# Kernel tuning notes

Measured on AMD Instinct MI355X. Metric: run time of the kernel, lower is better.

The kernel has to match this reference:

```python
import jax, jax.numpy as jnp
import numpy as np

C_IN = 64
C_QK = C_IN // 8  # 8


def setup_inputs() -> dict:
    key = jax.random.key(0)
    ks = jax.random.split(key, 8)
    B, C, D, H, W = 2, C_IN, 8, 32, 32
    x = jax.random.normal(ks[0], (B, C, D, H, W), dtype=jnp.float32)
    s = 1.0 / np.sqrt(C)
    Wq = jax.random.normal(ks[1], (C_QK, C), dtype=jnp.float32) * s
    bq = jax.random.normal(ks[2], (C_QK,), dtype=jnp.float32) * 0.01
    Wk = jax.random.normal(ks[3], (C_QK, C), dtype=jnp.float32) * s
    bk = jax.random.normal(ks[4], (C_QK,), dtype=jnp.float32) * 0.01
    Wv = jax.random.normal(ks[5], (C, C), dtype=jnp.float32) * s
    bv = jax.random.normal(ks[6], (C,), dtype=jnp.float32) * 0.01
    gamma = jax.random.normal(ks[7], (1,), dtype=jnp.float32) * 0.1
    return {"x": x, "Wq": Wq, "bq": bq, "Wk": Wk, "bk": bk,
            "Wv": Wv, "bv": bv, "gamma": gamma}


def reference(x, Wq, bq, Wk, bk, Wv, bv, gamma):
    B, C, D, H, W = x.shape
    N = D * H * W
    xf = x.reshape(B, C, N)  # flatten spatial dims (D,H,W order)
    # 1x1x1 conv3d == per-position channel matmul
    q = jnp.einsum('oc,bcn->bno', Wq, xf) + bq            # [B, N, Cqk]
    k = jnp.einsum('oc,bcn->bon', Wk, xf) + bk[:, None]   # [B, Cqk, N]
    v = jnp.einsum('oc,bcn->bon', Wv, xf) + bv[:, None]   # [B, C, N]
    energy = jnp.einsum('bnc,bcm->bnm', q, k)             # [B, N, N] (unscaled)
    attn = jax.nn.softmax(energy, axis=-1)
    # out[b,c,m] = sum_n v[b,c,n] * attn[b,m,n]  (bmm with attention^T)
    out = jnp.einsum('bcn,bmn->bcm', v, attn)
    out = out.reshape(B, C, D, H, W)
    return gamma[0] * out + x
```

## Files before the change

### kernel.cpp

```cpp
#include <hip/hip_runtime.h>
#include <hip/hip_bf16.h>
#include <math.h>

#define NPOS 8192
#define CIN 64
#define CQK 8
#define NB 2
#define LOG2E 1.4426950408889634f
#define SOFF 16.0f

typedef __attribute__((ext_vector_type(8))) short bf16x8;
typedef __attribute__((ext_vector_type(16))) float f32x16;

__device__ __forceinline__ unsigned short f2bf(float f) {
  union { float f; unsigned int u; } a; a.f = f;
  unsigned int r = a.u + 0x7FFFu + ((a.u >> 16) & 1u);
  return (unsigned short)(r >> 16);
}

__global__ __launch_bounds__(256) void qkv_proj(
    const float* __restrict__ x,
    const float* __restrict__ Wq, const float* __restrict__ bq,
    const float* __restrict__ Wk, const float* __restrict__ bk,
    const float* __restrict__ Wv, const float* __restrict__ bv,
    unsigned short* __restrict__ Qb, unsigned short* __restrict__ Kb,
    unsigned short* __restrict__ VB) {
  __shared__ float sWq[CQK * CIN], sWk[CQK * CIN], sWv[CIN * CIN], sb[2 * CQK + CIN];
  __shared__ unsigned short sV[64][66];
  int t = threadIdx.x;
  for (int i = t; i < CQK * CIN; i += 256) { sWq[i] = Wq[i] * LOG2E; sWk[i] = Wk[i]; }
  for (int i = t; i < CIN * CIN; i += 256) sWv[i] = Wv[i];
  if (t < CQK) sb[t] = bq[t] * LOG2E;
  if (t >= CQK && t < 2 * CQK) sb[t] = bk[t - CQK];
  if (t >= 2 * CQK && t < 2 * CQK + CIN) sb[t] = bv[t - 2 * CQK];
  __syncthreads();

  int p_loc = t & 63, grp = t >> 6;
  int gid = blockIdx.x * 64 + p_loc;
  int b = gid >> 13;
  int n = gid & (NPOS - 1);
  const float* xp = x + (size_t)b * CIN * NPOS + n;
  float xv[CIN];
#pragma unroll
  for (int c = 0; c < CIN; ++c) xv[c] = xp[(size_t)c * NPOS];

#pragma unroll
  for (int e = 0; e < 2; ++e) {
    int o = grp * 2 + e;
    float aq = sb[o], ak = sb[CQK + o];
    const float4* wq4 = (const float4*)&sWq[o * CIN];
    const float4* wk4 = (const float4*)&sWk[o * CIN];
#pragma unroll
    for (int c4 = 0; c4 < 16; ++c4) {
      float4 wq = wq4[c4], wk = wk4[c4];
      float x0 = xv[4 * c4], x1 = xv[4 * c4 + 1], x2 = xv[4 * c4 + 2], x3 = xv[4 * c4 + 3];
      aq += wq.x * x0 + wq.y * x1 + wq.z * x2 + wq.w * x3;
      ak += wk.x * x0 + wk.y * x1 + wk.z * x2 + wk.w * x3;
    }
    Qb[(size_t)gid * CQK + o] = f2bf(aq);
    Kb[(size_t)gid * CQK + o] = f2bf(ak);
  }
  for (int oo = 0; oo < 16; ++oo) {
    int o = grp * 16 + oo;
    float av = sb[2 * CQK + o];
    const float4* wv4 = (const float4*)&sWv[o * CIN];
#pragma unroll
    for (int c4 = 0; c4 < 16; ++c4) {
      float4 w = wv4[c4];
      av += w.x * xv[4 * c4] + w.y * xv[4 * c4 + 1] + w.z * xv[4 * c4 + 2] + w.w * xv[4 * c4 + 3];
    }
    sV[p_loc][o] = f2bf(av);
  }
  __syncthreads();

  int gid0 = blockIdx.x * 64;
  int bb = gid0 >> 13;
  int jb0 = (gid0 & (NPOS - 1)) >> 5;
  for (int cc = t; cc < 512; cc += 256) {
    int jbl = cc >> 8;
    int rem = cc & 255;
    int f = rem >> 6;
    int ln = rem & 63;
    int ch = ((f >> 1) << 5) + (ln & 31);
    int w0 = ((f & 1) << 4) + (((ln >> 5) & 1) << 2);
    union { unsigned short s[8]; bf16x8 v; } ou;
#pragma unroll
    for (int i = 0; i < 8; ++i) {
      int p = (jbl << 5) + w0 + (i & 3) + (((i >> 2) & 1) << 3);
      ou.s[i] = sV[p][ch];
    }
    *reinterpret_cast<bf16x8*>(
        VB + (((size_t)bb * 256 + jb0 + jbl) * 2048 + (size_t)f * 512 + ln * 8)) = ou.v;
  }
}

__global__ __launch_bounds__(512, 2) void flash_attn(
    const unsigned short* __restrict__ Qb, const unsigned short* __restrict__ Kb,
    const unsigned short* __restrict__ VB, const float* __restrict__ x,
    const float* __restrict__ gamma, float* __restrict__ out) {
  int tid = threadIdx.x;
  int wave = tid >> 6, lane = tid & 63;
  int qcol = lane & 31, hi = lane >> 5;
  int blk = blockIdx.x;
  int b = blk >> 8, qt = blk & 255;
  int qbase = qt * 32;

  bf16x8 qfrag;
#pragma unroll
  for (int i = 0; i < 8; ++i) qfrag[i] = 0;
  if (!hi) qfrag = *reinterpret_cast<const bf16x8*>(
      Qb + ((size_t)b * NPOS + qbase + qcol) * CQK);

  f32x16 z;
#pragma unroll
  for (int i = 0; i < 16; ++i) z[i] = -SOFF;
  f32x16 acc0, acc1;
#pragma unroll
  for (int i = 0; i < 16; ++i) { acc0[i] = 0.f; acc1[i] = 0.f; }
  float l = 0.f;

  const unsigned short* Kp = Kb + (size_t)b * NPOS * CQK;
  const bf16x8* Vt = reinterpret_cast<const bf16x8*>(VB + (size_t)b * 256 * 2048);

  int jb0 = wave << 5;
  bf16x8 kcur;
#pragma unroll
  for (int i = 0; i < 8; ++i) kcur[i] = 0;
  if (!hi) kcur = *reinterpret_cast<const bf16x8*>(
      Kp + ((size_t)(jb0 << 5) + qcol) * CQK);

  for (int t = 0; t < 32; ++t) {
    const bf16x8* tile = Vt + (size_t)(jb0 + t) * 256;
    bf16x8 va0 = tile[lane];
    bf16x8 va1 = tile[64 + lane];
    bf16x8 vb0 = tile[128 + lane];
    bf16x8 vb1 = tile[192 + lane];

    f32x16 S = __builtin_amdgcn_mfma_f32_32x32x16_bf16(kcur, qfrag, z, 0, 0, 0);

    bf16x8 knx;
#pragma unroll
    for (int i = 0; i < 8; ++i) knx[i] = 0;
    {
      int jn = jb0 + ((t + 1) & 31);
      if (!hi) knx = *reinterpret_cast<const bf16x8*>(
          Kp + ((size_t)(jn << 5) + qcol) * CQK);
    }

    unsigned int pk[8];
    float ls0 = 0.f, ls1 = 0.f;
#pragma unroll
    for (int jj = 0; jj < 8; ++jj) {
      float pa = __builtin_amdgcn_exp2f(S[2 * jj]);
      float pb = __builtin_amdgcn_exp2f(S[2 * jj + 1]);
      ls0 += pa; ls1 += pb;
      pk[jj] = __builtin_amdgcn_perm(__float_as_uint(pb), __float_as_uint(pa), 0x07060302u);
    }
    l += ls0 + ls1;

    union { unsigned int ui[4]; bf16x8 v; } PA0, PA1;
    PA0.ui[0] = pk[0]; PA0.ui[1] = pk[1]; PA0.ui[2] = pk[2]; PA0.ui[3] = pk[3];
    PA1.ui[0] = pk[4]; PA1.ui[1] = pk[5]; PA1.ui[2] = pk[6]; PA1.ui[3] = pk[7];

    acc0 = __builtin_amdgcn_mfma_f32_32x32x16_bf16(va0, PA0.v, acc0, 0, 0, 0);
    acc0 = __builtin_amdgcn_mfma_f32_32x32x16_bf16(va1, PA1.v, acc0, 0, 0, 0);
    acc1 = __builtin_amdgcn_mfma_f32_32x32x16_bf16(vb0, PA0.v, acc1, 0, 0, 0);
    acc1 = __builtin_amdgcn_mfma_f32_32x32x16_bf16(vb1, PA1.v, acc1, 0, 0, 0);

    kcur = knx;
  }

  __shared__ float sL[8][32], sLinv[32];
  __shared__ float sacc[64][32];
  for (int i = tid; i < CIN * 32; i += 512) (&sacc[0][0])[i] = 0.f;
  float lp = l + __shfl_xor(l, 32);
  if (!hi) sL[wave][qcol] = lp;
  __syncthreads();
  if (tid < 32) {
    float L = 0.f;
    for (int w2 = 0; w2 < 8; ++w2) L += sL[w2][tid];
    sLinv[tid] = 1.0f / L;
  }
  __syncthreads();
  for (int w2 = 0; w2 < 8; ++w2) {
    if (wave == w2) {
#pragma unroll
      for (int r = 0; r < 16; ++r) {
        int c = (r & 3) + ((r >> 2) << 3) + (hi << 2);
        sacc[c][qcol]      += acc0[r];
        sacc[c + 32][qcol] += acc1[r];
      }
    }
    __syncthreads();
  }
  float g = gamma[0];
  for (int i = tid; i < CIN * 32; i += 512) {
    int c = i >> 5, q = i & 31;
    size_t idx = ((size_t)b * CIN + c) * NPOS + qbase + q;
    out[idx] = g * sacc[c][q] * sLinv[q] + x[idx];
  }
}

extern "C" void kernel_launch(void* const* d_in, const int* in_sizes, int n_in,
                              void* d_out, int out_size, void* d_ws, size_t ws_size,
                              hipStream_t stream) {
  const float* x     = (const float*)d_in[0];
  const float* Wq    = (const float*)d_in[1];
  const float* bq    = (const float*)d_in[2];
  const float* Wk    = (const float*)d_in[3];
  const float* bk    = (const float*)d_in[4];
  const float* Wv    = (const float*)d_in[5];
  const float* bv    = (const float*)d_in[6];
  const float* gamma = (const float*)d_in[7];
  float* out = (float*)d_out;

  unsigned short* Qb = (unsigned short*)d_ws;
  unsigned short* Kb = Qb + (size_t)NB * NPOS * CQK;
  unsigned short* VB = Kb + (size_t)NB * NPOS * CQK;

  qkv_proj<<<dim3(NB * NPOS / 64), dim3(256), 0, stream>>>(
      x, Wq, bq, Wk, bk, Wv, bv, Qb, Kb, VB);
  flash_attn<<<dim3(NB * NPOS / 32), dim3(512), 0, stream>>>(
      Qb, Kb, VB, x, gamma, out);
}
```

Measured before the change: 49.77 us.

## Process 64 queries per block, reusing K/V tiles across two query fragments

The attention kernel now handles 64 queries per block with 4 waves instead of 32 queries with 8 waves. Each loaded K and V tile feeds two query fragments, which halves global V traffic per query and doubles MFMA work per load. The cross-wave reduction is rewritten to use float4 stores into a transposed, padded shared buffer. The projection kernel moves to 512 threads, so each thread computes fewer output channels. The trade-offs are more accumulator registers per thread, which may lower occupancy, and half as many attention blocks.

```diff
diff --git a/kernel.cpp b/kernel.cpp
--- a/kernel.cpp
+++ b/kernel.cpp
@@ -18,7 +18,7 @@
   return (unsigned short)(r >> 16);
 }
 
-__global__ __launch_bounds__(256) void qkv_proj(
+__global__ __launch_bounds__(512, 2) void qkv_proj(
     const float* __restrict__ x,
     const float* __restrict__ Wq, const float* __restrict__ bq,
     const float* __restrict__ Wk, const float* __restrict__ bk,
@@ -28,8 +28,8 @@
   __shared__ float sWq[CQK * CIN], sWk[CQK * CIN], sWv[CIN * CIN], sb[2 * CQK + CIN];
   __shared__ unsigned short sV[64][66];
   int t = threadIdx.x;
-  for (int i = t; i < CQK * CIN; i += 256) { sWq[i] = Wq[i] * LOG2E; sWk[i] = Wk[i]; }
-  for (int i = t; i < CIN * CIN; i += 256) sWv[i] = Wv[i];
+  for (int i = t; i < CQK * CIN; i += 512) { sWq[i] = Wq[i] * LOG2E; sWk[i] = Wk[i]; }
+  for (int i = t; i < CIN * CIN; i += 512) sWv[i] = Wv[i];
   if (t < CQK) sb[t] = bq[t] * LOG2E;
   if (t >= CQK && t < 2 * CQK) sb[t] = bk[t - CQK];
   if (t >= 2 * CQK && t < 2 * CQK + CIN) sb[t] = bv[t - 2 * CQK];
@@ -44,9 +44,8 @@
 #pragma unroll
   for (int c = 0; c < CIN; ++c) xv[c] = xp[(size_t)c * NPOS];
 
-#pragma unroll
-  for (int e = 0; e < 2; ++e) {
-    int o = grp * 2 + e;
+  {
+    int o = grp;
     float aq = sb[o], ak = sb[CQK + o];
     const float4* wq4 = (const float4*)&sWq[o * CIN];
     const float4* wk4 = (const float4*)&sWk[o * CIN];
@@ -60,8 +59,9 @@
     Qb[(size_t)gid * CQK + o] = f2bf(aq);
     Kb[(size_t)gid * CQK + o] = f2bf(ak);
   }
-  for (int oo = 0; oo < 16; ++oo) {
-    int o = grp * 16 + oo;
+#pragma unroll
+  for (int oo = 0; oo < 8; ++oo) {
+    int o = grp * 8 + oo;
     float av = sb[2 * CQK + o];
     const float4* wv4 = (const float4*)&sWv[o * CIN];
 #pragma unroll
@@ -76,7 +76,8 @@
   int gid0 = blockIdx.x * 64;
   int bb = gid0 >> 13;
   int jb0 = (gid0 & (NPOS - 1)) >> 5;
-  for (int cc = t; cc < 512; cc += 256) {
+  {
+    int cc = t;
     int jbl = cc >> 8;
     int rem = cc & 255;
     int f = rem >> 6;
@@ -94,7 +95,7 @@
   }
 }
 
-__global__ __launch_bounds__(512, 2) void flash_attn(
+__global__ __launch_bounds__(256, 2) void flash_attn(
     const unsigned short* __restrict__ Qb, const unsigned short* __restrict__ Kb,
     const unsigned short* __restrict__ VB, const float* __restrict__ x,
     const float* __restrict__ gamma, float* __restrict__ out) {
@@ -102,102 +103,130 @@
   int wave = tid >> 6, lane = tid & 63;
   int qcol = lane & 31, hi = lane >> 5;
   int blk = blockIdx.x;
-  int b = blk >> 8, qt = blk & 255;
-  int qbase = qt * 32;
-
-  bf16x8 qfrag;
-#pragma unroll
-  for (int i = 0; i < 8; ++i) qfrag[i] = 0;
-  if (!hi) qfrag = *reinterpret_cast<const bf16x8*>(
-      Qb + ((size_t)b * NPOS + qbase + qcol) * CQK);
+  int b = blk >> 7, qt = blk & 127;
+  int qbase = qt * 64;
+
+  bf16x8 qfrag0, qfrag1;
+#pragma unroll
+  for (int i = 0; i < 8; ++i) { qfrag0[i] = 0; qfrag1[i] = 0; }
+  if (!hi) {
+    qfrag0 = *reinterpret_cast<const bf16x8*>(Qb + ((size_t)b * NPOS + qbase + qcol) * CQK);
+    qfrag1 = *reinterpret_cast<const bf16x8*>(Qb + ((size_t)b * NPOS + qbase + 32 + qcol) * CQK);
+  }
 
   f32x16 z;
 #pragma unroll
   for (int i = 0; i < 16; ++i) z[i] = -SOFF;
-  f32x16 acc0, acc1;
-#pragma unroll
-  for (int i = 0; i < 16; ++i) { acc0[i] = 0.f; acc1[i] = 0.f; }
-  float l = 0.f;
+  f32x16 accA0, accB0, accA1, accB1;
+#pragma unroll
+  for (int i = 0; i < 16; ++i) { accA0[i] = 0.f; accB0[i] = 0.f; accA1[i] = 0.f; accB1[i] = 0.f; }
+  float l0 = 0.f, l1 = 0.f;
 
   const unsigned short* Kp = Kb + (size_t)b * NPOS * CQK;
   const bf16x8* Vt = reinterpret_cast<const bf16x8*>(VB + (size_t)b * 256 * 2048);
 
-  int jb0 = wave << 5;
+  int jb0 = wave << 6;
   bf16x8 kcur;
 #pragma unroll
   for (int i = 0; i < 8; ++i) kcur[i] = 0;
-  if (!hi) kcur = *reinterpret_cast<const bf16x8*>(
-      Kp + ((size_t)(jb0 << 5) + qcol) * CQK);
-
-  for (int t = 0; t < 32; ++t) {
-    const bf16x8* tile = Vt + (size_t)(jb0 + t) * 256;
+  if (!hi) kcur = *reinterpret_cast<const bf16x8*>(Kp + ((size_t)(jb0 << 5) + qcol) * CQK);
+
+  for (int tt = 0; tt < 64; ++tt) {
+    const bf16x8* tile = Vt + (size_t)(jb0 + tt) * 256;
     bf16x8 va0 = tile[lane];
     bf16x8 va1 = tile[64 + lane];
     bf16x8 vb0 = tile[128 + lane];
     bf16x8 vb1 = tile[192 + lane];
 
-    f32x16 S = __builtin_amdgcn_mfma_f32_32x32x16_bf16(kcur, qfrag, z, 0, 0, 0);
+    f32x16 S0 = __builtin_amdgcn_mfma_f32_32x32x16_bf16(kcur, qfrag0, z, 0, 0, 0);
+    f32x16 S1 = __builtin_amdgcn_mfma_f32_32x32x16_bf16(kcur, qfrag1, z, 0, 0, 0);
 
     bf16x8 knx;
 #pragma unroll
     for (int i = 0; i < 8; ++i) knx[i] = 0;
     {
-      int jn = jb0 + ((t + 1) & 31);
-      if (!hi) knx = *reinterpret_cast<const bf16x8*>(
-          Kp + ((size_t)(jn << 5) + qcol) * CQK);
-    }
-
-    unsigned int pk[8];
-    float ls0 = 0.f, ls1 = 0.f;
+      int jn = jb0 + ((tt + 1) & 63);
+      if (!hi) knx = *reinterpret_cast<const bf16x8*>(Kp + ((size_t)(jn << 5) + qcol) * CQK);
+    }
+
+    unsigned int pk0[8], pk1[8];
+    float lsa = 0.f, lsb = 0.f, lsc = 0.f, lsd = 0.f;
 #pragma unroll
     for (int jj = 0; jj < 8; ++jj) {
-      float pa = __builtin_amdgcn_exp2f(S[2 * jj]);
-      float pb = __builtin_amdgcn_exp2f(S[2 * jj + 1]);
-      ls0 += pa; ls1 += pb;
-      pk[jj] = __builtin_amdgcn_perm(__float_as_uint(pb), __float_as_uint(pa), 0x07060302u);
-    }
-    l += ls0 + ls1;
-
-    union { unsigned int ui[4]; bf16x8 v; } PA0, PA1;
-    PA0.ui[0] = pk[0]; PA0.ui[1] = pk[1]; PA0.ui[2] = pk[2]; PA0.ui[3] = pk[3];
-    PA1.ui[0] = pk[4]; PA1.ui[1] = pk[5]; PA1.ui[2] = pk[6]; PA1.ui[3] = pk[7];
-
-    acc0 = __builtin_amdgcn_mfma_f32_32x32x16_bf16(va0, PA0.v, acc0, 0, 0, 0);
-    acc0 = __builtin_amdgcn_mfma_f32_32x32x16_bf16(va1, PA1.v, acc0, 0, 0, 0);
-    acc1 = __builtin_amdgcn_mfma_f32_32x32x16_bf16(vb0, PA0.v, acc1, 0, 0, 0);
-    acc1 = __builtin_amdgcn_mfma_f32_32x32x16_bf16(vb1, PA1.v, acc1, 0, 0, 0);
+      float pa = __builtin_amdgcn_exp2f(S0[2 * jj]);
+      float pb = __builtin_amdgcn_exp2f(S0[2 * jj + 1]);
+      float pc = __builtin_amdgcn_exp2f(S1[2 * jj]);
+      float pd = __builtin_amdgcn_exp2f(S1[2 * jj + 1]);
+      lsa += pa; lsb += pb; lsc += pc; lsd += pd;
+      pk0[jj] = __builtin_amdgcn_perm(__float_as_uint(pb), __float_as_uint(pa), 0x07060302u);
+      pk1[jj] = __builtin_amdgcn_perm(__float_as_uint(pd), __float_as_uint(pc), 0x07060302u);
+    }
+    l0 += lsa + lsb;
+    l1 += lsc + lsd;
+
+    union { unsigned int ui[4]; bf16x8 v; } PA00, PA10, PA01, PA11;
+    PA00.ui[0] = pk0[0]; PA00.ui[1] = pk0[1]; PA00.ui[2] = pk0[2]; PA00.ui[3] = pk0[3];
+    PA10.ui[0] = pk0[4]; PA10.ui[1] = pk0[5]; PA10.ui[2] = pk0[6]; PA10.ui[3] = pk0[7];
+    PA01.ui[0] = pk1[0]; PA01.ui[1] = pk1[1]; PA01.ui[2] = pk1[2]; PA01.ui[3] = pk1[3];
+    PA11.ui[0] = pk1[4]; PA11.ui[1] = pk1[5]; PA11.ui[2] = pk1[6]; PA11.ui[3] = pk1[7];
+
+    accA0 = __builtin_amdgcn_mfma_f32_32x32x16_bf16(va0, PA00.v, accA0, 0, 0, 0);
+    accA0 = __builtin_amdgcn_mfma_f32_32x32x16_bf16(va1, PA10.v, accA0, 0, 0, 0);
+    accB0 = __builtin_amdgcn_mfma_f32_32x32x16_bf16(vb0, PA00.v, accB0, 0, 0, 0);
+    accB0 = __builtin_amdgcn_mfma_f32_32x32x16_bf16(vb1, PA10.v, accB0, 0, 0, 0);
+    accA1 = __builtin_amdgcn_mfma_f32_32x32x16_bf16(va0, PA01.v, accA1, 0, 0, 0);
+    accA1 = __builtin_amdgcn_mfma_f32_32x32x16_bf16(va1, PA11.v, accA1, 0, 0, 0);
+    accB1 = __builtin_amdgcn_mfma_f32_32x32x16_bf16(vb0, PA01.v, accB1, 0, 0, 0);
+    accB1 = __builtin_amdgcn_mfma_f32_32x32x16_bf16(vb1, PA11.v, accB1, 0, 0, 0);
 
     kcur = knx;
   }
 
-  __shared__ float sL[8][32], sLinv[32];
-  __shared__ float sacc[64][32];
-  for (int i = tid; i < CIN * 32; i += 512) (&sacc[0][0])[i] = 0.f;
-  float lp = l + __shfl_xor(l, 32);
-  if (!hi) sL[wave][qcol] = lp;
-  __syncthreads();
-  if (tid < 32) {
-    float L = 0.f;
-    for (int w2 = 0; w2 < 8; ++w2) L += sL[w2][tid];
+  __shared__ float sL[4][64];
+  __shared__ float sLinv[64];
+  __shared__ float sacc[64][68];
+  float lp0 = l0 + __shfl_xor(l0, 32);
+  float lp1 = l1 + __shfl_xor(l1, 32);
+  if (!hi) { sL[wave][qcol] = lp0; sL[wave][32 + qcol] = lp1; }
+  __syncthreads();
+  if (tid < 64) {
+    float L = sL[0][tid] + sL[1][tid] + sL[2][tid] + sL[3][tid];
     sLinv[tid] = 1.0f / L;
   }
-  __syncthreads();
-  for (int w2 = 0; w2 < 8; ++w2) {
+
+  for (int w2 = 0; w2 < 4; ++w2) {
+    __syncthreads();
     if (wave == w2) {
 #pragma unroll
-      for (int r = 0; r < 16; ++r) {
-        int c = (r & 3) + ((r >> 2) << 3) + (hi << 2);
-        sacc[c][qcol]      += acc0[r];
-        sacc[c + 32][qcol] += acc1[r];
+      for (int k = 0; k < 4; ++k) {
+        int c0 = (k << 3) + (hi << 2);
+        float4 cA0 = make_float4(accA0[4 * k], accA0[4 * k + 1], accA0[4 * k + 2], accA0[4 * k + 3]);
+        float4 cB0 = make_float4(accB0[4 * k], accB0[4 * k + 1], accB0[4 * k + 2], accB0[4 * k + 3]);
+        float4 cA1 = make_float4(accA1[4 * k], accA1[4 * k + 1], accA1[4 * k + 2], accA1[4 * k + 3]);
+        float4 cB1 = make_float4(accB1[4 * k], accB1[4 * k + 1], accB1[4 * k + 2], accB1[4 * k + 3]);
+        float4* pA0 = (float4*)&sacc[qcol][c0];
+        float4* pB0 = (float4*)&sacc[qcol][c0 + 32];
+        float4* pA1 = (float4*)&sacc[32 + qcol][c0];
+        float4* pB1 = (float4*)&sacc[32 + qcol][c0 + 32];
+        if (w2 == 0) { *pA0 = cA0; *pB0 = cB0; *pA1 = cA1; *pB1 = cB1; }
+        else {
+          float4 a = *pA0, bq_ = *pB0, c = *pA1, d = *pB1;
+          a.x += cA0.x; a.y += cA0.y; a.z += cA0.z; a.w += cA0.w;
+          bq_.x += cB0.x; bq_.y += cB0.y; bq_.z += cB0.z; bq_.w += cB0.w;
+          c.x += cA1.x; c.y += cA1.y; c.z += cA1.z; c.w += cA1.w;
+          d.x += cB1.x; d.y += cB1.y; d.z += cB1.z; d.w += cB1.w;
+          *pA0 = a; *pB0 = bq_; *pA1 = c; *pB1 = d;
+        }
       }
     }
-    __syncthreads();
-  }
+  }
+  __syncthreads();
+
   float g = gamma[0];
-  for (int i = tid; i < CIN * 32; i += 512) {
-    int c = i >> 5, q = i & 31;
+  for (int i = tid; i < CIN * 64; i += 256) {
+    int c = i >> 6, q = i & 63;
     size_t idx = ((size_t)b * CIN + c) * NPOS + qbase + q;
-    out[idx] = g * sacc[c][q] * sLinv[q] + x[idx];
+    out[idx] = g * sacc[q][c] * sLinv[q] + x[idx];
   }
 }
 
@@ -218,8 +247,8 @@
   unsigned short* Kb = Qb + (size_t)NB * NPOS * CQK;
   unsigned short* VB = Kb + (size_t)NB * NPOS * CQK;
 
-  qkv_proj<<<dim3(NB * NPOS / 64), dim3(256), 0, stream>>>(
+  qkv_proj<<<dim3(NB * NPOS / 64), dim3(512), 0, stream>>>(
       x, Wq, bq, Wk, bk, Wv, bv, Qb, Kb, VB);
-  flash_attn<<<dim3(NB * NPOS / 32), dim3(512), 0, stream>>>(
+  flash_attn<<<dim3(NB * NPOS / 64), dim3(256), 0, stream>>>(
       Qb, Kb, VB, x, gamma, out);
 }
```

After: 47.18 us. 5.2% less time.

## Split attention over key ranges with LDS-staged shared K/V and a merge kernel

Applied to the files above, without the earlier changes.

The attention kernel now assigns 256 queries per block (32 per wave) and splits the key dimension into four chunks across blocks. K and V tiles are staged into LDS with global_load_lds double buffering, so all eight waves share each tile instead of each wave reading its own. Partial unnormalized outputs and row sums go to a workspace, and a new merge kernel sums them, normalizes, and applies the gamma residual. The projection kernel also switches to 32 positions per block. The cost is extra global traffic for the partials, a third launch, and per-step block barriers.

```diff
diff --git a/kernel.cpp b/kernel.cpp
--- a/kernel.cpp
+++ b/kernel.cpp
@@ -8,9 +8,15 @@
 #define NB 2
 #define LOG2E 1.4426950408889634f
 #define SOFF 16.0f
+#define KSPL 4
+#define KH (NPOS / KSPL)
+#define STEPS (KH / 64)
 
 typedef __attribute__((ext_vector_type(8))) short bf16x8;
 typedef __attribute__((ext_vector_type(16))) float f32x16;
+
+typedef __attribute__((address_space(3))) void lds_void;
+typedef __attribute__((address_space(1))) const void glb_void;
 
 __device__ __forceinline__ unsigned short f2bf(float f) {
   union { float f; unsigned int u; } a; a.f = f;
@@ -18,7 +24,7 @@
   return (unsigned short)(r >> 16);
 }
 
-__global__ __launch_bounds__(256) void qkv_proj(
+__global__ __launch_bounds__(256, 2) void qkv_proj(
     const float* __restrict__ x,
     const float* __restrict__ Wq, const float* __restrict__ bq,
     const float* __restrict__ Wk, const float* __restrict__ bk,
@@ -26,7 +32,7 @@
     unsigned short* __restrict__ Qb, unsigned short* __restrict__ Kb,
     unsigned short* __restrict__ VB) {
   __shared__ float sWq[CQK * CIN], sWk[CQK * CIN], sWv[CIN * CIN], sb[2 * CQK + CIN];
-  __shared__ unsigned short sV[64][66];
+  __shared__ unsigned short sV[32][66];
   int t = threadIdx.x;
   for (int i = t; i < CQK * CIN; i += 256) { sWq[i] = Wq[i] * LOG2E; sWk[i] = Wk[i]; }
   for (int i = t; i < CIN * CIN; i += 256) sWv[i] = Wv[i];
@@ -35,8 +41,8 @@
   if (t >= 2 * CQK && t < 2 * CQK + CIN) sb[t] = bv[t - 2 * CQK];
   __syncthreads();
 
-  int p_loc = t & 63, grp = t >> 6;
-  int gid = blockIdx.x * 64 + p_loc;
+  int p_loc = t & 31, grp = t >> 5;
+  int gid = blockIdx.x * 32 + p_loc;
   int b = gid >> 13;
   int n = gid & (NPOS - 1);
   const float* xp = x + (size_t)b * CIN * NPOS + n;
@@ -44,9 +50,8 @@
 #pragma unroll
   for (int c = 0; c < CIN; ++c) xv[c] = xp[(size_t)c * NPOS];
 
-#pragma unroll
-  for (int e = 0; e < 2; ++e) {
-    int o = grp * 2 + e;
+  {
+    int o = grp;
     float aq = sb[o], ak = sb[CQK + o];
     const float4* wq4 = (const float4*)&sWq[o * CIN];
     const float4* wk4 = (const float4*)&sWk[o * CIN];
@@ -60,8 +65,9 @@
     Qb[(size_t)gid * CQK + o] = f2bf(aq);
     Kb[(size_t)gid * CQK + o] = f2bf(ak);
   }
-  for (int oo = 0; oo < 16; ++oo) {
-    int o = grp * 16 + oo;
+#pragma unroll
+  for (int oo = 0; oo < 8; ++oo) {
+    int o = grp * 8 + oo;
     float av = sb[2 * CQK + o];
     const float4* wv4 = (const float4*)&sWv[o * CIN];
 #pragma unroll
@@ -73,43 +79,46 @@
   }
   __syncthreads();
 
-  int gid0 = blockIdx.x * 64;
-  int bb = gid0 >> 13;
-  int jb0 = (gid0 & (NPOS - 1)) >> 5;
-  for (int cc = t; cc < 512; cc += 256) {
-    int jbl = cc >> 8;
-    int rem = cc & 255;
-    int f = rem >> 6;
-    int ln = rem & 63;
+  {
+    int gid0 = blockIdx.x * 32;
+    int bb = gid0 >> 13;
+    int jb = (gid0 & (NPOS - 1)) >> 5;
+    int f = t >> 6;
+    int ln = t & 63;
     int ch = ((f >> 1) << 5) + (ln & 31);
     int w0 = ((f & 1) << 4) + (((ln >> 5) & 1) << 2);
     union { unsigned short s[8]; bf16x8 v; } ou;
 #pragma unroll
     for (int i = 0; i < 8; ++i) {
-      int p = (jbl << 5) + w0 + (i & 3) + (((i >> 2) & 1) << 3);
+      int p = w0 + (i & 3) + (((i >> 2) & 1) << 3);
       ou.s[i] = sV[p][ch];
     }
     *reinterpret_cast<bf16x8*>(
-        VB + (((size_t)bb * 256 + jb0 + jbl) * 2048 + (size_t)f * 512 + ln * 8)) = ou.v;
+        VB + (((size_t)bb * 256 + jb) * 2048 + (size_t)f * 512 + ln * 8)) = ou.v;
   }
 }
 
 __global__ __launch_bounds__(512, 2) void flash_attn(
     const unsigned short* __restrict__ Qb, const unsigned short* __restrict__ Kb,
-    const unsigned short* __restrict__ VB, const float* __restrict__ x,
-    const float* __restrict__ gamma, float* __restrict__ out) {
+    const unsigned short* __restrict__ VB,
+    float* __restrict__ Opart, float* __restrict__ lpart) {
+  __shared__ unsigned short sbuf[2][4608];
+  __shared__ float sep[8][64][33];
+
   int tid = threadIdx.x;
   int wave = tid >> 6, lane = tid & 63;
   int qcol = lane & 31, hi = lane >> 5;
   int blk = blockIdx.x;
-  int b = blk >> 8, qt = blk & 255;
-  int qbase = qt * 32;
+  int qb = blk >> 2, ks = blk & 3;
+  int b = qb >> 5;
+  int kbase = ks * KH;
+  int jbBase = (ks * KH) >> 5;
 
   bf16x8 qfrag;
 #pragma unroll
   for (int i = 0; i < 8; ++i) qfrag[i] = 0;
   if (!hi) qfrag = *reinterpret_cast<const bf16x8*>(
-      Qb + ((size_t)b * NPOS + qbase + qcol) * CQK);
+      Qb + ((size_t)qb * 256 + wave * 32 + qcol) * CQK);
 
   f32x16 z;
 #pragma unroll
@@ -120,84 +129,106 @@
   float l = 0.f;
 
   const unsigned short* Kp = Kb + (size_t)b * NPOS * CQK;
-  const bf16x8* Vt = reinterpret_cast<const bf16x8*>(VB + (size_t)b * 256 * 2048);
-
-  int jb0 = wave << 5;
-  bf16x8 kcur;
-#pragma unroll
-  for (int i = 0; i < 8; ++i) kcur[i] = 0;
-  if (!hi) kcur = *reinterpret_cast<const bf16x8*>(
-      Kp + ((size_t)(jb0 << 5) + qcol) * CQK);
-
-  for (int t = 0; t < 32; ++t) {
-    const bf16x8* tile = Vt + (size_t)(jb0 + t) * 256;
-    bf16x8 va0 = tile[lane];
-    bf16x8 va1 = tile[64 + lane];
-    bf16x8 vb0 = tile[128 + lane];
-    bf16x8 vb1 = tile[192 + lane];
-
-    f32x16 S = __builtin_amdgcn_mfma_f32_32x32x16_bf16(kcur, qfrag, z, 0, 0, 0);
-
-    bf16x8 knx;
-#pragma unroll
-    for (int i = 0; i < 8; ++i) knx[i] = 0;
-    {
-      int jn = jb0 + ((t + 1) & 31);
-      if (!hi) knx = *reinterpret_cast<const bf16x8*>(
-          Kp + ((size_t)(jn << 5) + qcol) * CQK);
-    }
-
-    unsigned int pk[8];
-    float ls0 = 0.f, ls1 = 0.f;
-#pragma unroll
-    for (int jj = 0; jj < 8; ++jj) {
-      float pa = __builtin_amdgcn_exp2f(S[2 * jj]);
-      float pb = __builtin_amdgcn_exp2f(S[2 * jj + 1]);
-      ls0 += pa; ls1 += pb;
-      pk[jj] = __builtin_amdgcn_perm(__float_as_uint(pb), __float_as_uint(pa), 0x07060302u);
-    }
-    l += ls0 + ls1;
-
-    union { unsigned int ui[4]; bf16x8 v; } PA0, PA1;
-    PA0.ui[0] = pk[0]; PA0.ui[1] = pk[1]; PA0.ui[2] = pk[2]; PA0.ui[3] = pk[3];
-    PA1.ui[0] = pk[4]; PA1.ui[1] = pk[5]; PA1.ui[2] = pk[6]; PA1.ui[3] = pk[7];
-
-    acc0 = __builtin_amdgcn_mfma_f32_32x32x16_bf16(va0, PA0.v, acc0, 0, 0, 0);
-    acc0 = __builtin_amdgcn_mfma_f32_32x32x16_bf16(va1, PA1.v, acc0, 0, 0, 0);
-    acc1 = __builtin_amdgcn_mfma_f32_32x32x16_bf16(vb0, PA0.v, acc1, 0, 0, 0);
-    acc1 = __builtin_amdgcn_mfma_f32_32x32x16_bf16(vb1, PA1.v, acc1, 0, 0, 0);
-
-    kcur = knx;
-  }
-
-  __shared__ float sL[8][32], sLinv[32];
-  __shared__ float sacc[64][32];
-  for (int i = tid; i < CIN * 32; i += 512) (&sacc[0][0])[i] = 0.f;
-  float lp = l + __shfl_xor(l, 32);
-  if (!hi) sL[wave][qcol] = lp;
+  const unsigned short* VBb = VB + (size_t)b * 256 * 2048;
+
+  auto stage = [&](int buf, int step) {
+    const unsigned short* vsrc =
+        VBb + ((size_t)(jbBase + step * 2)) * 2048 + wave * 512 + lane * 8;
+    __builtin_amdgcn_global_load_lds((glb_void*)vsrc,
+                                     (lds_void*)&sbuf[buf][wave * 512], 16, 0, 0);
+    if (wave == 0) {
+      const unsigned short* ksrc = Kp + ((size_t)(kbase + step * 64)) * CQK + lane * 8;
+      __builtin_amdgcn_global_load_lds((glb_void*)ksrc,
+                                       (lds_void*)&sbuf[buf][4096], 16, 0, 0);
+    }
+  };
+
+  stage(0, 0);
   __syncthreads();
-  if (tid < 32) {
-    float L = 0.f;
-    for (int w2 = 0; w2 < 8; ++w2) L += sL[w2][tid];
-    sLinv[tid] = 1.0f / L;
-  }
-  __syncthreads();
-  for (int w2 = 0; w2 < 8; ++w2) {
-    if (wave == w2) {
-#pragma unroll
-      for (int r = 0; r < 16; ++r) {
-        int c = (r & 3) + ((r >> 2) << 3) + (hi << 2);
-        sacc[c][qcol]      += acc0[r];
-        sacc[c + 32][qcol] += acc1[r];
+
+  for (int step = 0; step < STEPS; ++step) {
+    int cur = step & 1;
+    if (step + 1 < STEPS) stage(cur ^ 1, step + 1);
+
+#pragma unroll
+    for (int u = 0; u < 2; ++u) {
+      bf16x8 kfrag = *reinterpret_cast<const bf16x8*>(
+          &sbuf[cur][4096 + u * 256 + qcol * 8]);
+      f32x16 S = __builtin_amdgcn_mfma_f32_32x32x16_bf16(kfrag, qfrag, z, 0, 0, 0);
+
+      const unsigned short* vb = &sbuf[cur][u * 2048];
+      bf16x8 va0 = *reinterpret_cast<const bf16x8*>(vb + (size_t)lane * 8);
+      bf16x8 va1 = *reinterpret_cast<const bf16x8*>(vb + 512 + (size_t)lane * 8);
+      bf16x8 vb0 = *reinterpret_cast<const bf16x8*>(vb + 1024 + (size_t)lane * 8);
+      bf16x8 vb1 = *reinterpret_cast<const bf16x8*>(vb + 1536 + (size_t)lane * 8);
+
+      unsigned int pk[8];
+      float ls0 = 0.f, ls1 = 0.f;
+#pragma unroll
+      for (int jj = 0; jj < 8; ++jj) {
+        float pa = __builtin_amdgcn_exp2f(S[2 * jj]);
+        float pb = __builtin_amdgcn_exp2f(S[2 * jj + 1]);
+        ls0 += pa; ls1 += pb;
+        pk[jj] = __builtin_amdgcn_perm(__float_as_uint(pb), __float_as_uint(pa),
+                                       0x07060302u);
       }
+      l += ls0 + ls1;
+
+      union { unsigned int ui[4]; bf16x8 v; } PA0, PA1;
+      PA0.ui[0] = pk[0]; PA0.ui[1] = pk[1]; PA0.ui[2] = pk[2]; PA0.ui[3] = pk[3];
+      PA1.ui[0] = pk[4]; PA1.ui[1] = pk[5]; PA1.ui[2] = pk[6]; PA1.ui[3] = pk[7];
+
+      acc0 = __builtin_amdgcn_mfma_f32_32x32x16_bf16(va0, PA0.v, acc0, 0, 0, 0);
+      acc0 = __builtin_amdgcn_mfma_f32_32x32x16_bf16(va1, PA1.v, acc0, 0, 0, 0);
+      acc1 = __builtin_amdgcn_mfma_f32_32x32x16_bf16(vb0, PA0.v, acc1, 0, 0, 0);
+      acc1 = __builtin_amdgcn_mfma_f32_32x32x16_bf16(vb1, PA1.v, acc1, 0, 0, 0);
     }
     __syncthreads();
   }
-  float g = gamma[0];
-  for (int i = tid; i < CIN * 32; i += 512) {
-    int c = i >> 5, q = i & 31;
-    size_t idx = ((size_t)b * CIN + c) * NPOS + qbase + q;
-    out[idx] = g * sacc[c][q] * sLinv[q] + x[idx];
+
+  float l2 = l + __shfl_xor(l, 32);
+  if (!hi) lpart[((qb << 2) + ks) * 256 + wave * 32 + qcol] = l2;
+
+#pragma unroll
+  for (int r = 0; r < 16; ++r) {
+    int c0 = (r & 3) + ((r >> 2) << 3) + (hi << 2);
+    sep[wave][c0][qcol] = acc0[r];
+    sep[wave][c0 + 32][qcol] = acc1[r];
+  }
+  float* Ob = Opart + (((size_t)(qb << 2) + ks) << 6) * 256;
+#pragma unroll
+  for (int cc = 0; cc < 32; ++cc) {
+    int c = (cc << 1) | hi;
+    Ob[(size_t)c * 256 + wave * 32 + qcol] = sep[wave][c][qcol];
+  }
+}
+
+__global__ __launch_bounds__(256) void pam_merge(
+    const float* __restrict__ Opart, const float* __restrict__ lpart,
+    const float* __restrict__ x, const float* __restrict__ gamma,
+    float* __restrict__ out) {
+  int blk = blockIdx.x;
+  int qb = blk >> 3, oct = blk & 7;
+  int t = threadIdx.x;
+  int ql = oct * 32 + (t & 31);
+  int cg = t >> 5;
+  int gq = qb * 256 + ql;
+  int b = gq >> 13, pos = gq & (NPOS - 1);
+
+  float L = 0.f;
+#pragma unroll
+  for (int ksv = 0; ksv < KSPL; ++ksv) L += lpart[((qb << 2) + ksv) * 256 + ql];
+  float gi = gamma[0] / L;
+
+#pragma unroll
+  for (int j = 0; j < 8; ++j) {
+    int c = cg * 8 + j;
+    float s = 0.f;
+#pragma unroll
+    for (int ksv = 0; ksv < KSPL; ++ksv)
+      s += Opart[((((size_t)(qb << 2) + ksv) << 6) + c) * 256 + ql];
+    size_t oidx = ((size_t)(b * CIN + c)) * NPOS + pos;
+    out[oidx] = s * gi + x[oidx];
   }
 }
 
@@ -214,12 +245,15 @@
   const float* gamma = (const float*)d_in[7];
   float* out = (float*)d_out;
 
-  unsigned short* Qb = (unsigned short*)d_ws;
-  unsigned short* Kb = Qb + (size_t)NB * NPOS * CQK;
-  unsigned short* VB = Kb + (size_t)NB * NPOS * CQK;
-
-  qkv_proj<<<dim3(NB * NPOS / 64), dim3(256), 0, stream>>>(
+  char* ws = (char*)d_ws;
+  unsigned short* Qb = (unsigned short*)(ws);
+  unsigned short* Kb = (unsigned short*)(ws + (256 << 10));
+  unsigned short* VB = (unsigned short*)(ws + (512 << 10));
+  float* Opart = (float*)(ws + (4 << 20));
+  float* lpart = (float*)(ws + (20 << 20));
+
+  qkv_proj<<<dim3(NB * NPOS / 32), dim3(256), 0, stream>>>(
       x, Wq, bq, Wk, bk, Wv, bv, Qb, Kb, VB);
-  flash_attn<<<dim3(NB * NPOS / 32), dim3(512), 0, stream>>>(
-      Qb, Kb, VB, x, gamma, out);
-}
+  flash_attn<<<dim3(64 * KSPL), dim3(512), 0, stream>>>(Qb, Kb, VB, Opart, lpart);
+  pam_merge<<<dim3(64 * 8), dim3(256), 0, stream>>>(Opart, lpart, x, gamma, out);
+}
```

Measured after the change: 58.29 us. 1.17x slower.

## Restructure QKV projection and attention epilogue, relax flash-attention launch bounds

Applied to the files above, without the earlier changes.

The projection kernel now runs 512 threads per block, one wave per Q/K output channel. Weights are read directly from global memory with wave-uniform indices, which replaces the shared-memory staging and its barrier. In the attention kernel, the K-fragment loads drop the upper-half-lane mask, since those lanes pair with zeroed Q anyway. The cross-wave accumulator reduction now writes float4 rows into a transposed, padded shared buffer, so the zero-initialisation pass is skipped. The minimum-blocks hint of 2 per CU is removed from launch bounds, which may let the compiler use more registers at the cost of occupancy.

```diff
diff --git a/kernel.cpp b/kernel.cpp
--- a/kernel.cpp
+++ b/kernel.cpp
@@ -18,25 +18,18 @@
   return (unsigned short)(r >> 16);
 }
 
-__global__ __launch_bounds__(256) void qkv_proj(
+__global__ __launch_bounds__(512) void qkv_proj(
     const float* __restrict__ x,
     const float* __restrict__ Wq, const float* __restrict__ bq,
     const float* __restrict__ Wk, const float* __restrict__ bk,
     const float* __restrict__ Wv, const float* __restrict__ bv,
     unsigned short* __restrict__ Qb, unsigned short* __restrict__ Kb,
     unsigned short* __restrict__ VB) {
-  __shared__ float sWq[CQK * CIN], sWk[CQK * CIN], sWv[CIN * CIN], sb[2 * CQK + CIN];
   __shared__ unsigned short sV[64][66];
-  int t = threadIdx.x;
-  for (int i = t; i < CQK * CIN; i += 256) { sWq[i] = Wq[i] * LOG2E; sWk[i] = Wk[i]; }
-  for (int i = t; i < CIN * CIN; i += 256) sWv[i] = Wv[i];
-  if (t < CQK) sb[t] = bq[t] * LOG2E;
-  if (t >= CQK && t < 2 * CQK) sb[t] = bk[t - CQK];
-  if (t >= 2 * CQK && t < 2 * CQK + CIN) sb[t] = bv[t - 2 * CQK];
-  __syncthreads();
-
-  int p_loc = t & 63, grp = t >> 6;
-  int gid = blockIdx.x * 64 + p_loc;
+  int tid = threadIdx.x;
+  int wave = __builtin_amdgcn_readfirstlane(tid >> 6);
+  int lane = tid & 63;
+  int gid = blockIdx.x * 64 + lane;
   int b = gid >> 13;
   int n = gid & (NPOS - 1);
   const float* xp = x + (size_t)b * CIN * NPOS + n;
@@ -44,39 +37,36 @@
 #pragma unroll
   for (int c = 0; c < CIN; ++c) xv[c] = xp[(size_t)c * NPOS];
 
-#pragma unroll
-  for (int e = 0; e < 2; ++e) {
-    int o = grp * 2 + e;
-    float aq = sb[o], ak = sb[CQK + o];
-    const float4* wq4 = (const float4*)&sWq[o * CIN];
-    const float4* wk4 = (const float4*)&sWk[o * CIN];
-#pragma unroll
-    for (int c4 = 0; c4 < 16; ++c4) {
-      float4 wq = wq4[c4], wk = wk4[c4];
-      float x0 = xv[4 * c4], x1 = xv[4 * c4 + 1], x2 = xv[4 * c4 + 2], x3 = xv[4 * c4 + 3];
-      aq += wq.x * x0 + wq.y * x1 + wq.z * x2 + wq.w * x3;
-      ak += wk.x * x0 + wk.y * x1 + wk.z * x2 + wk.w * x3;
-    }
-    Qb[(size_t)gid * CQK + o] = f2bf(aq);
-    Kb[(size_t)gid * CQK + o] = f2bf(ak);
-  }
-  for (int oo = 0; oo < 16; ++oo) {
-    int o = grp * 16 + oo;
-    float av = sb[2 * CQK + o];
-    const float4* wv4 = (const float4*)&sWv[o * CIN];
-#pragma unroll
-    for (int c4 = 0; c4 < 16; ++c4) {
-      float4 w = wv4[c4];
-      av += w.x * xv[4 * c4] + w.y * xv[4 * c4 + 1] + w.z * xv[4 * c4 + 2] + w.w * xv[4 * c4 + 3];
-    }
-    sV[p_loc][o] = f2bf(av);
+  {
+    const float* wq = Wq + wave * CIN;
+    const float* wk = Wk + wave * CIN;
+    float aq = 0.f, ak = 0.f;
+#pragma unroll
+    for (int c = 0; c < CIN; ++c) {
+      aq += wq[c] * xv[c];
+      ak += wk[c] * xv[c];
+    }
+    aq = (aq + bq[wave]) * LOG2E;
+    ak += bk[wave];
+    Qb[(size_t)gid * CQK + wave] = f2bf(aq);
+    Kb[(size_t)gid * CQK + wave] = f2bf(ak);
+  }
+#pragma unroll
+  for (int oo = 0; oo < 8; ++oo) {
+    int o = wave * 8 + oo;
+    const float* wv = Wv + o * CIN;
+    float av = bv[o];
+#pragma unroll
+    for (int c = 0; c < CIN; ++c) av += wv[c] * xv[c];
+    sV[lane][o] = f2bf(av);
   }
   __syncthreads();
 
-  int gid0 = blockIdx.x * 64;
-  int bb = gid0 >> 13;
-  int jb0 = (gid0 & (NPOS - 1)) >> 5;
-  for (int cc = t; cc < 512; cc += 256) {
+  {
+    int gid0 = blockIdx.x * 64;
+    int bb = gid0 >> 13;
+    int jb0 = (gid0 & (NPOS - 1)) >> 5;
+    int cc = tid;
     int jbl = cc >> 8;
     int rem = cc & 255;
     int f = rem >> 6;
@@ -94,7 +84,7 @@
   }
 }
 
-__global__ __launch_bounds__(512, 2) void flash_attn(
+__global__ __launch_bounds__(512) void flash_attn(
     const unsigned short* __restrict__ Qb, const unsigned short* __restrict__ Kb,
     const unsigned short* __restrict__ VB, const float* __restrict__ x,
     const float* __restrict__ gamma, float* __restrict__ out) {
@@ -123,14 +113,10 @@
   const bf16x8* Vt = reinterpret_cast<const bf16x8*>(VB + (size_t)b * 256 * 2048);
 
   int jb0 = wave << 5;
-  bf16x8 kcur;
-#pragma unroll
-  for (int i = 0; i < 8; ++i) kcur[i] = 0;
-  if (!hi) kcur = *reinterpret_cast<const bf16x8*>(
-      Kp + ((size_t)(jb0 << 5) + qcol) * CQK);
-
-  for (int t = 0; t < 32; ++t) {
-    const bf16x8* tile = Vt + (size_t)(jb0 + t) * 256;
+  bf16x8 kcur = *reinterpret_cast<const bf16x8*>(Kp + ((size_t)(jb0 << 5) + qcol) * CQK);
+
+  for (int tt = 0; tt < 32; ++tt) {
+    const bf16x8* tile = Vt + (size_t)(jb0 + tt) * 256;
     bf16x8 va0 = tile[lane];
     bf16x8 va1 = tile[64 + lane];
     bf16x8 vb0 = tile[128 + lane];
@@ -138,14 +124,8 @@
 
     f32x16 S = __builtin_amdgcn_mfma_f32_32x32x16_bf16(kcur, qfrag, z, 0, 0, 0);
 
-    bf16x8 knx;
-#pragma unroll
-    for (int i = 0; i < 8; ++i) knx[i] = 0;
-    {
-      int jn = jb0 + ((t + 1) & 31);
-      if (!hi) knx = *reinterpret_cast<const bf16x8*>(
-          Kp + ((size_t)(jn << 5) + qcol) * CQK);
-    }
+    int jn = jb0 + ((tt + 1) & 31);
+    bf16x8 knx = *reinterpret_cast<const bf16x8*>(Kp + ((size_t)(jn << 5) + qcol) * CQK);
 
     unsigned int pk[8];
     float ls0 = 0.f, ls1 = 0.f;
@@ -170,34 +150,46 @@
     kcur = knx;
   }
 
-  __shared__ float sL[8][32], sLinv[32];
-  __shared__ float sacc[64][32];
-  for (int i = tid; i < CIN * 32; i += 512) (&sacc[0][0])[i] = 0.f;
+  __shared__ float sL[8][32];
+  __shared__ float sLinv[32];
+  __shared__ float sacc[32][68];
   float lp = l + __shfl_xor(l, 32);
   if (!hi) sL[wave][qcol] = lp;
   __syncthreads();
   if (tid < 32) {
     float L = 0.f;
+#pragma unroll
     for (int w2 = 0; w2 < 8; ++w2) L += sL[w2][tid];
     sLinv[tid] = 1.0f / L;
   }
+
+  for (int w2 = 0; w2 < 8; ++w2) {
+    __syncthreads();
+    if (wave == w2) {
+#pragma unroll
+      for (int k = 0; k < 4; ++k) {
+        int c0 = (k << 3) + (hi << 2);
+        float4 cA = make_float4(acc0[4 * k], acc0[4 * k + 1], acc0[4 * k + 2], acc0[4 * k + 3]);
+        float4 cB = make_float4(acc1[4 * k], acc1[4 * k + 1], acc1[4 * k + 2], acc1[4 * k + 3]);
+        float4* pA = (float4*)&sacc[qcol][c0];
+        float4* pB = (float4*)&sacc[qcol][c0 + 32];
+        if (w2 == 0) { *pA = cA; *pB = cB; }
+        else {
+          float4 a = *pA, bb = *pB;
+          a.x += cA.x; a.y += cA.y; a.z += cA.z; a.w += cA.w;
+          bb.x += cB.x; bb.y += cB.y; bb.z += cB.z; bb.w += cB.w;
+          *pA = a; *pB = bb;
+        }
+      }
+    }
+  }
   __syncthreads();
-  for (int w2 = 0; w2 < 8; ++w2) {
-    if (wave == w2) {
-#pragma unroll
-      for (int r = 0; r < 16; ++r) {
-        int c = (r & 3) + ((r >> 2) << 3) + (hi << 2);
-        sacc[c][qcol]      += acc0[r];
-        sacc[c + 32][qcol] += acc1[r];
-      }
-    }
-    __syncthreads();
-  }
+
   float g = gamma[0];
   for (int i = tid; i < CIN * 32; i += 512) {
     int c = i >> 5, q = i & 31;
     size_t idx = ((size_t)b * CIN + c) * NPOS + qbase + q;
-    out[idx] = g * sacc[c][q] * sLinv[q] + x[idx];
+    out[idx] = g * sacc[q][c] * sLinv[q] + x[idx];
   }
 }
 
@@ -218,7 +210,7 @@
   unsigned short* Kb = Qb + (size_t)NB * NPOS * CQK;
   unsigned short* VB = Kb + (size_t)NB * NPOS * CQK;
 
-  qkv_proj<<<dim3(NB * NPOS / 64), dim3(256), 0, stream>>>(
+  qkv_proj<<<dim3(NB * NPOS / 64), dim3(512), 0, stream>>>(
       x, Wq, bq, Wk, bk, Wv, bv, Qb, Kb, VB);
   flash_attn<<<dim3(NB * NPOS / 32), dim3(512), 0, stream>>>(
       Qb, Kb, VB, x, gamma, out);
```

New measurement: 50.44 us. Within noise of the previous version (+1.3%).
